# Performance work log

Measured on AMD Instinct MI355X. Metric: run time of the kernel, lower is better.

## Reference

```python
import jax, jax.numpy as jnp
import numpy as np

B, S, INP, HID = 64, 2048, 512, 512

def setup_inputs() -> dict:
    key = jax.random.key(0)
    ks = jax.random.split(key, 8)
    inp = jax.random.normal(ks[0], (B, INP), dtype=jnp.float32)
    context = jax.random.normal(ks[1], (B, S, INP), dtype=jnp.float32)
    mask = jax.random.randint(ks[2], (B, S), 0, 2) == 1  # True = masked out
    lim_l = 1.0 / np.sqrt(INP)
    Wl = jax.random.uniform(ks[3], (HID, INP), minval=-lim_l, maxval=lim_l, dtype=jnp.float32)
    bl = jax.random.uniform(ks[4], (HID,), minval=-lim_l, maxval=lim_l, dtype=jnp.float32)
    Wc = jax.random.uniform(ks[5], (HID, INP), minval=-lim_l, maxval=lim_l, dtype=jnp.float32)  # Conv1d k=1 weight squeezed
    bc = jax.random.uniform(ks[6], (HID,), minval=-lim_l, maxval=lim_l, dtype=jnp.float32)
    V = jax.random.uniform(ks[7], (HID,), minval=-1.0, maxval=1.0, dtype=jnp.float32)
    return {"inp": inp, "context": context, "mask": mask,
            "Wl": Wl, "bl": bl, "Wc": Wc, "bc": bc, "V": V}

def reference(inp, context, mask, Wl, bl, Wc, bc, V):
    # hid: [B, HID], broadcast over S
    hid = inp @ Wl.T + bl
    # 1x1 Conv1d over permuted context == per-position linear: [B, HID, S]
    ctx = jnp.einsum('bsi,hi->bhs', context, Wc) + bc[None, :, None]
    # additive attention scores: [B, S]
    att = jnp.einsum('h,bhs->bs', V, jnp.tanh(hid[:, :, None] + ctx))
    att = jnp.where(mask, -jnp.inf, att)
    alpha = jax.nn.softmax(att, axis=1)
    # context vector: [B, HID]
    hidden_state = jnp.einsum('bhs,bs->bh', ctx, alpha)
    return (hidden_state, alpha)
```

## Files before the change

kernel.cpp:

```cpp
#include <hip/hip_runtime.h>
#include <hip/hip_bf16.h>
#include <cstdint>
#include <cstddef>

#define B_   64
#define S_   2048
#define INP_ 512
#define HID_ 512

typedef float          floatx4  __attribute__((ext_vector_type(4)));
typedef __bf16         bf16x8   __attribute__((ext_vector_type(8)));
typedef unsigned short ushortx8 __attribute__((ext_vector_type(8)));
typedef unsigned short ushortx4 __attribute__((ext_vector_type(4)));

__device__ __forceinline__ unsigned short f2bf(float f) {
  unsigned u = __float_as_uint(f);
  u += 0x7FFFu + ((u >> 16) & 1u);
  return (unsigned short)(u >> 16);
}
__device__ __forceinline__ float bf2f(unsigned short h) {
  return __uint_as_float(((unsigned)h) << 16);
}
__device__ __forceinline__ float fast_tanh(float x) {
  float u = __builtin_amdgcn_exp2f(x * 2.88539008177792681472f);
  return 1.0f - 2.0f * __builtin_amdgcn_rcpf(u + 1.0f);
}

__global__ void hid_kernel(const float* __restrict__ inp, const float* __restrict__ Wl,
                           const float* __restrict__ bl, float* __restrict__ hid)
{
  __shared__ float ism[512];
  const int b = blockIdx.x, t = threadIdx.x;
  ism[t]       = inp[b * 512 + t];
  ism[t + 256] = inp[b * 512 + 256 + t];
  __syncthreads();
  #pragma unroll
  for (int hh = 0; hh < 2; ++hh) {
    int h = t + hh * 256;
    const float4* wr = (const float4*)(Wl + (size_t)h * 512);
    float4 sv = {0.f, 0.f, 0.f, 0.f};
    for (int i = 0; i < 128; ++i) {
      float4 wv = wr[i];
      float4 iv = *(const float4*)(&ism[i * 4]);
      sv.x += wv.x * iv.x; sv.y += wv.y * iv.y;
      sv.z += wv.z * iv.z; sv.w += wv.w * iv.w;
    }
    hid[b * 512 + h] = bl[h] + sv.x + sv.y + sv.z + sv.w;
  }
}

__global__ void pack_wc_kernel(const float* __restrict__ Wc, unsigned short* __restrict__ pk)
{
  int g = blockIdx.x * 256 + threadIdx.x;
  int l = g & 63, ks = (g >> 6) & 15, m16 = g >> 10;
  int row = m16 * 16 + (l & 15);
  int kb  = ks * 32 + (l >> 4) * 8;
  const float4* s = (const float4*)(Wc + (size_t)row * 512 + kb);
  float4 a = s[0], c = s[1];
  ushortx8 o = { f2bf(a.x), f2bf(a.y), f2bf(a.z), f2bf(a.w),
                 f2bf(c.x), f2bf(c.y), f2bf(c.z), f2bf(c.w) };
  *(ushortx8*)(pk + (size_t)g * 8) = o;
}

template<int MODE>
__global__ __launch_bounds__(256, 2) void ctx_gemm_kernel(
    const float* __restrict__ context, const unsigned short* __restrict__ Wc_pk,
    const float* __restrict__ hid, const float* __restrict__ bc,
    const float* __restrict__ V,
    unsigned short* __restrict__ ctx_out, float* __restrict__ att,
    const float* __restrict__ alpha, float* __restrict__ hidden)
{
  __shared__ alignas(16) unsigned short bsm[64 * 128];
  __shared__ float hid_sm[512];
  __shared__ float V_sm[512];
  __shared__ float bc_sm[512];
  __shared__ float att_sm[64];
  __shared__ float alpha_sm[64];

  const int b    = blockIdx.y;
  const int s0   = blockIdx.x * 64;
  const int t    = threadIdx.x;
  const int lane = t & 63;
  const int w    = t >> 6;
  const int quad = lane >> 4;
  const int l15  = lane & 15;

  for (int i = t; i < 512; i += 256) {
    hid_sm[i] = hid[b * 512 + i];
    V_sm[i]   = V[i];
    bc_sm[i]  = bc[i];
  }
  if (t < 64) {
    att_sm[t] = 0.0f;
    if (MODE == 2) alpha_sm[t] = alpha[b * S_ + s0 + t];
  }

  floatx4 acc[8][4];
  #pragma unroll
  for (int m = 0; m < 8; ++m)
    #pragma unroll
    for (int n = 0; n < 4; ++n) { floatx4 z = {0.f,0.f,0.f,0.f}; acc[m][n] = z; }

  const unsigned short* apBase = Wc_pk + (size_t)(w * 8) * 8192 + lane * 8;
  const float* src = context + ((size_t)b * S_ + s0) * INP_;

  for (int phase = 0; phase < 4; ++phase) {
    __syncthreads();
    #pragma unroll
    for (int i = 0; i < 8; ++i) {
      int id  = t + i * 256;
      int row = id >> 5;
      int c4  = id & 31;
      float4 f = *(const float4*)(src + (size_t)row * INP_ + phase * 128 + c4 * 4);
      int chunk = c4 >> 1, half = c4 & 1;
      int sw = chunk ^ (row & 7);
      ushortx4 hv = { f2bf(f.x), f2bf(f.y), f2bf(f.z), f2bf(f.w) };
      *(ushortx4*)(&bsm[row * 128 + sw * 8 + half * 4]) = hv;
    }
    __syncthreads();
    #pragma unroll
    for (int ksl = 0; ksl < 4; ++ksl) {
      const int ksg = phase * 4 + ksl;
      bf16x8 af[8];
      #pragma unroll
      for (int m = 0; m < 8; ++m)
        af[m] = *(const bf16x8*)(apBase + (size_t)m * 8192 + ksg * 512);
      bf16x8 bfr[4];
      #pragma unroll
      for (int n = 0; n < 4; ++n) {
        int row = n * 16 + l15;
        int c   = ksl * 4 + quad;
        bfr[n] = *(const bf16x8*)(&bsm[row * 128 + ((c ^ (row & 7)) * 8)]);
      }
      #pragma unroll
      for (int m = 0; m < 8; ++m)
        #pragma unroll
        for (int n = 0; n < 4; ++n)
          acc[m][n] = __builtin_amdgcn_mfma_f32_16x16x32_bf16(af[m], bfr[n], acc[m][n], 0, 0, 0);
    }
  }

  if (MODE == 0 || MODE == 1) {
    float attacc[4] = {0.f, 0.f, 0.f, 0.f};
    #pragma unroll
    for (int m = 0; m < 8; ++m) {
      int hb = w * 128 + m * 16 + quad * 4;
      #pragma unroll
      for (int r = 0; r < 4; ++r) {
        int h = hb + r;
        float bcv = bc_sm[h], hv = hid_sm[h], vv = V_sm[h];
        #pragma unroll
        for (int n = 0; n < 4; ++n) {
          float val = acc[m][n][r] + bcv;
          if (MODE == 0)
            ctx_out[((size_t)b * HID_ + h) * S_ + s0 + n * 16 + l15] = f2bf(val);
          attacc[n] += vv * fast_tanh(hv + val);
        }
      }
    }
    #pragma unroll
    for (int n = 0; n < 4; ++n) {
      float v = attacc[n];
      v += __shfl_xor(v, 16);
      v += __shfl_xor(v, 32);
      if (lane < 16) atomicAdd(&att_sm[n * 16 + l15], v);
    }
    __syncthreads();
    if (t < 64) att[b * S_ + s0 + t] = att_sm[t];
  } else {
    #pragma unroll
    for (int m = 0; m < 8; ++m) {
      int hb = w * 128 + m * 16 + quad * 4;
      #pragma unroll
      for (int r = 0; r < 4; ++r) {
        int h = hb + r;
        float bcv = bc_sm[h];
        float hacc = 0.0f;
        #pragma unroll
        for (int n = 0; n < 4; ++n)
          hacc += (acc[m][n][r] + bcv) * alpha_sm[n * 16 + l15];
        hacc += __shfl_xor(hacc, 1);
        hacc += __shfl_xor(hacc, 2);
        hacc += __shfl_xor(hacc, 4);
        hacc += __shfl_xor(hacc, 8);
        if (l15 == 0) atomicAdd(&hidden[b * HID_ + h], hacc);
      }
    }
  }
}

__global__ void softmax_kernel(const void* __restrict__ mask,
                               const float* __restrict__ att,
                               float* __restrict__ alpha)
{
  __shared__ int flags;
  __shared__ float red[8];
  const int b = blockIdx.x, t = threadIdx.x;
  const int lane = t & 63, w = t >> 6;
  if (t == 0) flags = 0;
  __syncthreads();
  int f = 0;
  const unsigned* mw = (const unsigned*)mask;
  for (int i = t; i < 512; i += 256) {
    unsigned v = mw[i];
    if (v > 1u) f |= 1;
    if (v != 0u && v != 0x3f800000u) f |= 2;
  }
  if (f) atomicOr(&flags, f);
  __syncthreads();
  const int fl = flags;
  const int mode = ((fl & 1) == 0) ? 0 : (((fl & 2) == 0) ? 1 : 2);

  float v[8]; bool msk[8];
  float vmax = -1e30f;
  #pragma unroll
  for (int i = 0; i < 8; ++i) {
    int idx = i * 256 + t;
    bool m;
    if (mode == 0)      m = ((const int*)mask)[b * S_ + idx] != 0;
    else if (mode == 1) m = ((const float*)mask)[b * S_ + idx] != 0.0f;
    else                m = ((const unsigned char*)mask)[b * S_ + idx] != 0;
    msk[i] = m;
    v[i] = att[b * S_ + idx];
    if (!m) vmax = fmaxf(vmax, v[i]);
  }
  #pragma unroll
  for (int off = 32; off; off >>= 1) vmax = fmaxf(vmax, __shfl_xor(vmax, off));
  if (lane == 0) red[w] = vmax;
  __syncthreads();
  vmax = fmaxf(fmaxf(red[0], red[1]), fmaxf(red[2], red[3]));

  float e[8], s = 0.0f;
  #pragma unroll
  for (int i = 0; i < 8; ++i) {
    e[i] = msk[i] ? 0.0f : __builtin_amdgcn_exp2f((v[i] - vmax) * 1.4426950408889634f);
    s += e[i];
  }
  #pragma unroll
  for (int off = 32; off; off >>= 1) s += __shfl_xor(s, off);
  if (lane == 0) red[4 + w] = s;
  __syncthreads();
  s = red[4] + red[5] + red[6] + red[7];
  float rinv = 1.0f / s;
  #pragma unroll
  for (int i = 0; i < 8; ++i)
    alpha[b * S_ + i * 256 + t] = e[i] * rinv;
}

__global__ void hidden_kernel(const unsigned short* __restrict__ ctx,
                              const float* __restrict__ alpha,
                              float* __restrict__ hidden)
{
  const int b = blockIdx.y;
  const int w = threadIdx.x >> 6, lane = threadIdx.x & 63;
  const int h = blockIdx.x * 4 + w;
  const unsigned short* cp = ctx + ((size_t)b * HID_ + h) * S_;
  const float* ap = alpha + (size_t)b * S_;
  float acc = 0.0f;
  #pragma unroll
  for (int it = 0; it < 4; ++it) {
    int s = it * 512 + lane * 8;
    ushortx8 cv = *(const ushortx8*)(cp + s);
    float4 a0 = *(const float4*)(ap + s);
    float4 a1 = *(const float4*)(ap + s + 4);
    acc += bf2f(cv[0]) * a0.x + bf2f(cv[1]) * a0.y + bf2f(cv[2]) * a0.z + bf2f(cv[3]) * a0.w
         + bf2f(cv[4]) * a1.x + bf2f(cv[5]) * a1.y + bf2f(cv[6]) * a1.z + bf2f(cv[7]) * a1.w;
  }
  #pragma unroll
  for (int off = 32; off; off >>= 1) acc += __shfl_xor(acc, off);
  if (lane == 0) hidden[b * HID_ + h] = acc;
}

extern "C" void kernel_launch(void* const* d_in, const int* in_sizes, int n_in,
                              void* d_out, int out_size, void* d_ws, size_t ws_size,
                              hipStream_t stream)
{
  const float* inp     = (const float*)d_in[0];
  const float* context = (const float*)d_in[1];
  const void*  mask    = d_in[2];
  const float* Wl      = (const float*)d_in[3];
  const float* bl      = (const float*)d_in[4];
  const float* Wc      = (const float*)d_in[5];
  const float* bc      = (const float*)d_in[6];
  const float* V       = (const float*)d_in[7];

  float* hidden = (float*)d_out;
  float* alpha  = (float*)d_out + B_ * HID_;

  char* ws = (char*)d_ws;
  const size_t CTX_BYTES = (size_t)B_ * HID_ * S_ * 2;
  const size_t HIDW_BYTES = (size_t)B_ * HID_ * 4;
  const size_t ATT_BYTES  = (size_t)B_ * S_ * 4;
  const size_t PK_BYTES   = (size_t)HID_ * INP_ * 2;
  const bool big = ws_size >= CTX_BYTES + HIDW_BYTES + ATT_BYTES + PK_BYTES;

  if (big) {
    unsigned short* ctx_bf = (unsigned short*)ws;
    float* hid_ws          = (float*)(ws + CTX_BYTES);
    float* att_ws          = (float*)(ws + CTX_BYTES + HIDW_BYTES);
    unsigned short* pk     = (unsigned short*)(ws + CTX_BYTES + HIDW_BYTES + ATT_BYTES);

    hid_kernel<<<B_, 256, 0, stream>>>(inp, Wl, bl, hid_ws);
    pack_wc_kernel<<<128, 256, 0, stream>>>(Wc, pk);
    ctx_gemm_kernel<0><<<dim3(S_ / 64, B_), 256, 0, stream>>>(
        context, pk, hid_ws, bc, V, ctx_bf, att_ws, nullptr, nullptr);
    softmax_kernel<<<B_, 256, 0, stream>>>(mask, att_ws, alpha);
    hidden_kernel<<<dim3(HID_ / 4, B_), 256, 0, stream>>>(ctx_bf, alpha, hidden);
  } else {
    float* hid_ws      = (float*)ws;
    float* att_ws      = (float*)(ws + HIDW_BYTES);
    unsigned short* pk = (unsigned short*)(ws + HIDW_BYTES + ATT_BYTES);

    hid_kernel<<<B_, 256, 0, stream>>>(inp, Wl, bl, hid_ws);
    pack_wc_kernel<<<128, 256, 0, stream>>>(Wc, pk);
    ctx_gemm_kernel<1><<<dim3(S_ / 64, B_), 256, 0, stream>>>(
        context, pk, hid_ws, bc, V, nullptr, att_ws, nullptr, nullptr);
    softmax_kernel<<<B_, 256, 0, stream>>>(mask, att_ws, alpha);
    hipMemsetAsync(hidden, 0, HIDW_BYTES, stream);
    ctx_gemm_kernel<2><<<dim3(S_ / 64, B_), 256, 0, stream>>>(
        context, pk, hid_ws, bc, V, nullptr, nullptr, alpha, hidden);
  }
}
```

Baseline: 518.3 us.

## Reassociate hidden-state as Wc·(context·alpha) and load context via LDS DMA

Uses linearity to compute hidden = Wc·(Σ_s alpha_s·context_s) + bc, since alpha sums to one. A new cbar kernel computes the alpha-weighted context average in fp32 partial chunks, and a rowdot kernel then applies Wc plus bias. This removes the need to write and reread the full bf16 ctx tensor or rerun the GEMM. The attention GEMM now loads fp32 context straight into LDS with global_load_lds and converts to bf16 at fragment-read time; it also streams A fragments per m to cut register use. The costs are a doubled LDS footprint for the tile, which may lower occupancy, and a second full read of context.

```diff
diff --git a/kernel.cpp b/kernel.cpp
--- a/kernel.cpp
+++ b/kernel.cpp
@@ -11,41 +11,57 @@
 typedef float          floatx4  __attribute__((ext_vector_type(4)));
 typedef __bf16         bf16x8   __attribute__((ext_vector_type(8)));
 typedef unsigned short ushortx8 __attribute__((ext_vector_type(8)));
-typedef unsigned short ushortx4 __attribute__((ext_vector_type(4)));
 
 __device__ __forceinline__ unsigned short f2bf(float f) {
   unsigned u = __float_as_uint(f);
   u += 0x7FFFu + ((u >> 16) & 1u);
   return (unsigned short)(u >> 16);
 }
-__device__ __forceinline__ float bf2f(unsigned short h) {
-  return __uint_as_float(((unsigned)h) << 16);
-}
 __device__ __forceinline__ float fast_tanh(float x) {
   float u = __builtin_amdgcn_exp2f(x * 2.88539008177792681472f);
   return 1.0f - 2.0f * __builtin_amdgcn_rcpf(u + 1.0f);
 }
 
-__global__ void hid_kernel(const float* __restrict__ inp, const float* __restrict__ Wl,
-                           const float* __restrict__ bl, float* __restrict__ hid)
-{
-  __shared__ float ism[512];
-  const int b = blockIdx.x, t = threadIdx.x;
-  ism[t]       = inp[b * 512 + t];
-  ism[t + 256] = inp[b * 512 + 256 + t];
-  __syncthreads();
-  #pragma unroll
-  for (int hh = 0; hh < 2; ++hh) {
-    int h = t + hh * 256;
-    const float4* wr = (const float4*)(Wl + (size_t)h * 512);
-    float4 sv = {0.f, 0.f, 0.f, 0.f};
-    for (int i = 0; i < 128; ++i) {
-      float4 wv = wr[i];
-      float4 iv = *(const float4*)(&ism[i * 4]);
-      sv.x += wv.x * iv.x; sv.y += wv.y * iv.y;
-      sv.z += wv.z * iv.z; sv.w += wv.w * iv.w;
-    }
-    hid[b * 512 + h] = bl[h] + sv.x + sv.y + sv.z + sv.w;
+__device__ __forceinline__ void gload_lds16(const float* g, float* l) {
+  __builtin_amdgcn_global_load_lds(
+      (const __attribute__((address_space(1))) unsigned int*)(const void*)g,
+      (__attribute__((address_space(3))) unsigned int*)(void*)l, 16, 0, 0);
+}
+
+template<int NPART>
+__global__ __launch_bounds__(256) void rowdot_kernel(
+    const float* __restrict__ W, const float* __restrict__ bias,
+    const float* __restrict__ vecs, float* __restrict__ out, int nch)
+{
+  __shared__ float vs[512];
+  const int b = blockIdx.y, t = threadIdx.x;
+  const int w = t >> 6, lane = t & 63;
+  for (int i = t; i < 512; i += 256) {
+    float s;
+    if (NPART) {
+      s = 0.0f;
+      for (int c = 0; c < nch; ++c)
+        s += vecs[((size_t)c * B_ + b) * INP_ + i];
+    } else {
+      s = vecs[(size_t)b * 512 + i];
+    }
+    vs[i] = s;
+  }
+  __syncthreads();
+  float vl[8];
+  #pragma unroll
+  for (int j = 0; j < 8; ++j) vl[j] = vs[lane * 8 + j];
+  const int h0 = blockIdx.x * 64 + w * 16;
+  #pragma unroll
+  for (int i = 0; i < 16; ++i) {
+    const int h = h0 + i;
+    const float4* wr = (const float4*)(W + (size_t)h * 512 + lane * 8);
+    float4 w0 = wr[0], w1 = wr[1];
+    float d = w0.x*vl[0] + w0.y*vl[1] + w0.z*vl[2] + w0.w*vl[3]
+            + w1.x*vl[4] + w1.y*vl[5] + w1.z*vl[6] + w1.w*vl[7];
+    #pragma unroll
+    for (int off = 32; off; off >>= 1) d += __shfl_xor(d, off);
+    if (lane == 0) out[(size_t)b * 512 + h] = bias[h] + d;
   }
 }
 
@@ -62,20 +78,16 @@
   *(ushortx8*)(pk + (size_t)g * 8) = o;
 }
 
-template<int MODE>
-__global__ __launch_bounds__(256, 2) void ctx_gemm_kernel(
+__global__ __launch_bounds__(256, 2) void att_gemm_kernel(
     const float* __restrict__ context, const unsigned short* __restrict__ Wc_pk,
     const float* __restrict__ hid, const float* __restrict__ bc,
-    const float* __restrict__ V,
-    unsigned short* __restrict__ ctx_out, float* __restrict__ att,
-    const float* __restrict__ alpha, float* __restrict__ hidden)
-{
-  __shared__ alignas(16) unsigned short bsm[64 * 128];
+    const float* __restrict__ V, float* __restrict__ att)
+{
+  __shared__ alignas(16) float bsf[64 * 128];
   __shared__ float hid_sm[512];
   __shared__ float V_sm[512];
   __shared__ float bc_sm[512];
   __shared__ float att_sm[64];
-  __shared__ float alpha_sm[64];
 
   const int b    = blockIdx.y;
   const int s0   = blockIdx.x * 64;
@@ -90,10 +102,7 @@
     V_sm[i]   = V[i];
     bc_sm[i]  = bc[i];
   }
-  if (t < 64) {
-    att_sm[t] = 0.0f;
-    if (MODE == 2) alpha_sm[t] = alpha[b * S_ + s0 + t];
-  }
+  if (t < 64) att_sm[t] = 0.0f;
 
   floatx4 acc[8][4];
   #pragma unroll
@@ -108,85 +117,64 @@
     __syncthreads();
     #pragma unroll
     for (int i = 0; i < 8; ++i) {
-      int id  = t + i * 256;
-      int row = id >> 5;
-      int c4  = id & 31;
-      float4 f = *(const float4*)(src + (size_t)row * INP_ + phase * 128 + c4 * 4);
-      int chunk = c4 >> 1, half = c4 & 1;
-      int sw = chunk ^ (row & 7);
-      ushortx4 hv = { f2bf(f.x), f2bf(f.y), f2bf(f.z), f2bf(f.w) };
-      *(ushortx4*)(&bsm[row * 128 + sw * 8 + half * 4]) = hv;
+      const int row = (w * 8 + i) * 2 + (lane >> 5);
+      const int c   = (lane & 31) ^ (row & 7);
+      gload_lds16(src + (size_t)row * INP_ + phase * 128 + c * 4,
+                  &bsf[(w * 8 + i) * 256]);
     }
     __syncthreads();
     #pragma unroll
     for (int ksl = 0; ksl < 4; ++ksl) {
       const int ksg = phase * 4 + ksl;
-      bf16x8 af[8];
-      #pragma unroll
-      for (int m = 0; m < 8; ++m)
-        af[m] = *(const bf16x8*)(apBase + (size_t)m * 8192 + ksg * 512);
       bf16x8 bfr[4];
       #pragma unroll
       for (int n = 0; n < 4; ++n) {
-        int row = n * 16 + l15;
-        int c   = ksl * 4 + quad;
-        bfr[n] = *(const bf16x8*)(&bsm[row * 128 + ((c ^ (row & 7)) * 8)]);
+        const int row = n * 16 + l15;
+        const int cb  = ksl * 8 + quad * 2;
+        const int p0  = cb ^ (row & 7);
+        const int p1  = (cb + 1) ^ (row & 7);
+        floatx4 f0 = *(const floatx4*)(&bsf[row * 128 + p0 * 4]);
+        floatx4 f1 = *(const floatx4*)(&bsf[row * 128 + p1 * 4]);
+        bf16x8 r;
+        r[0] = (__bf16)f0[0]; r[1] = (__bf16)f0[1];
+        r[2] = (__bf16)f0[2]; r[3] = (__bf16)f0[3];
+        r[4] = (__bf16)f1[0]; r[5] = (__bf16)f1[1];
+        r[6] = (__bf16)f1[2]; r[7] = (__bf16)f1[3];
+        bfr[n] = r;
       }
       #pragma unroll
-      for (int m = 0; m < 8; ++m)
+      for (int m = 0; m < 8; ++m) {
+        bf16x8 af = *(const bf16x8*)(apBase + (size_t)m * 8192 + (size_t)ksg * 512);
         #pragma unroll
         for (int n = 0; n < 4; ++n)
-          acc[m][n] = __builtin_amdgcn_mfma_f32_16x16x32_bf16(af[m], bfr[n], acc[m][n], 0, 0, 0);
-    }
-  }
-
-  if (MODE == 0 || MODE == 1) {
-    float attacc[4] = {0.f, 0.f, 0.f, 0.f};
-    #pragma unroll
-    for (int m = 0; m < 8; ++m) {
-      int hb = w * 128 + m * 16 + quad * 4;
+          acc[m][n] = __builtin_amdgcn_mfma_f32_16x16x32_bf16(af, bfr[n], acc[m][n], 0, 0, 0);
+      }
+    }
+  }
+
+  float attacc[4] = {0.f, 0.f, 0.f, 0.f};
+  #pragma unroll
+  for (int m = 0; m < 8; ++m) {
+    const int hb = w * 128 + m * 16 + quad * 4;
+    #pragma unroll
+    for (int r = 0; r < 4; ++r) {
+      const int h = hb + r;
+      const float base = hid_sm[h] + bc_sm[h];
+      const float vv = V_sm[h];
       #pragma unroll
-      for (int r = 0; r < 4; ++r) {
-        int h = hb + r;
-        float bcv = bc_sm[h], hv = hid_sm[h], vv = V_sm[h];
-        #pragma unroll
-        for (int n = 0; n < 4; ++n) {
-          float val = acc[m][n][r] + bcv;
-          if (MODE == 0)
-            ctx_out[((size_t)b * HID_ + h) * S_ + s0 + n * 16 + l15] = f2bf(val);
-          attacc[n] += vv * fast_tanh(hv + val);
-        }
-      }
-    }
-    #pragma unroll
-    for (int n = 0; n < 4; ++n) {
-      float v = attacc[n];
-      v += __shfl_xor(v, 16);
-      v += __shfl_xor(v, 32);
-      if (lane < 16) atomicAdd(&att_sm[n * 16 + l15], v);
-    }
-    __syncthreads();
-    if (t < 64) att[b * S_ + s0 + t] = att_sm[t];
-  } else {
-    #pragma unroll
-    for (int m = 0; m < 8; ++m) {
-      int hb = w * 128 + m * 16 + quad * 4;
-      #pragma unroll
-      for (int r = 0; r < 4; ++r) {
-        int h = hb + r;
-        float bcv = bc_sm[h];
-        float hacc = 0.0f;
-        #pragma unroll
-        for (int n = 0; n < 4; ++n)
-          hacc += (acc[m][n][r] + bcv) * alpha_sm[n * 16 + l15];
-        hacc += __shfl_xor(hacc, 1);
-        hacc += __shfl_xor(hacc, 2);
-        hacc += __shfl_xor(hacc, 4);
-        hacc += __shfl_xor(hacc, 8);
-        if (l15 == 0) atomicAdd(&hidden[b * HID_ + h], hacc);
-      }
-    }
-  }
+      for (int n = 0; n < 4; ++n)
+        attacc[n] += vv * fast_tanh(base + acc[m][n][r]);
+    }
+  }
+  #pragma unroll
+  for (int n = 0; n < 4; ++n) {
+    float v = attacc[n];
+    v += __shfl_xor(v, 16);
+    v += __shfl_xor(v, 32);
+    if (lane < 16) atomicAdd(&att_sm[n * 16 + l15], v);
+  }
+  __syncthreads();
+  if (t < 64) att[b * S_ + s0 + t] = att_sm[t];
 }
 
 __global__ void softmax_kernel(const void* __restrict__ mask,
@@ -247,28 +235,26 @@
     alpha[b * S_ + i * 256 + t] = e[i] * rinv;
 }
 
-__global__ void hidden_kernel(const unsigned short* __restrict__ ctx,
-                              const float* __restrict__ alpha,
-                              float* __restrict__ hidden)
-{
-  const int b = blockIdx.y;
-  const int w = threadIdx.x >> 6, lane = threadIdx.x & 63;
-  const int h = blockIdx.x * 4 + w;
-  const unsigned short* cp = ctx + ((size_t)b * HID_ + h) * S_;
-  const float* ap = alpha + (size_t)b * S_;
-  float acc = 0.0f;
-  #pragma unroll
-  for (int it = 0; it < 4; ++it) {
-    int s = it * 512 + lane * 8;
-    ushortx8 cv = *(const ushortx8*)(cp + s);
-    float4 a0 = *(const float4*)(ap + s);
-    float4 a1 = *(const float4*)(ap + s + 4);
-    acc += bf2f(cv[0]) * a0.x + bf2f(cv[1]) * a0.y + bf2f(cv[2]) * a0.z + bf2f(cv[3]) * a0.w
-         + bf2f(cv[4]) * a1.x + bf2f(cv[5]) * a1.y + bf2f(cv[6]) * a1.z + bf2f(cv[7]) * a1.w;
-  }
-  #pragma unroll
-  for (int off = 32; off; off >>= 1) acc += __shfl_xor(acc, off);
-  if (lane == 0) hidden[b * HID_ + h] = acc;
+__global__ __launch_bounds__(256) void cbar_kernel(
+    const float* __restrict__ context, const float* __restrict__ alpha,
+    float* __restrict__ partial, int rows)
+{
+  __shared__ float a_sm[2048];
+  const int b = blockIdx.y, c = blockIdx.x, t = threadIdx.x;
+  const int s0 = c * rows;
+  for (int i = t; i < rows; i += 256) a_sm[i] = alpha[(size_t)b * S_ + s0 + i];
+  __syncthreads();
+  const float* base = context + ((size_t)b * S_ + s0) * INP_ + t * 2;
+  float ax = 0.f, ay = 0.f;
+  #pragma unroll 8
+  for (int s = 0; s < rows; ++s) {
+    float2 v = *(const float2*)(base + (size_t)s * INP_);
+    float a = a_sm[s];
+    ax = fmaf(a, v.x, ax);
+    ay = fmaf(a, v.y, ay);
+  }
+  float2 o; o.x = ax; o.y = ay;
+  *(float2*)(partial + ((size_t)c * B_ + b) * INP_ + t * 2) = o;
 }
 
 extern "C" void kernel_launch(void* const* d_in, const int* in_sizes, int n_in,
@@ -288,36 +274,24 @@
   float* alpha  = (float*)d_out + B_ * HID_;
 
   char* ws = (char*)d_ws;
-  const size_t CTX_BYTES = (size_t)B_ * HID_ * S_ * 2;
   const size_t HIDW_BYTES = (size_t)B_ * HID_ * 4;
   const size_t ATT_BYTES  = (size_t)B_ * S_ * 4;
   const size_t PK_BYTES   = (size_t)HID_ * INP_ * 2;
-  const bool big = ws_size >= CTX_BYTES + HIDW_BYTES + ATT_BYTES + PK_BYTES;
-
-  if (big) {
-    unsigned short* ctx_bf = (unsigned short*)ws;
-    float* hid_ws          = (float*)(ws + CTX_BYTES);
-    float* att_ws          = (float*)(ws + CTX_BYTES + HIDW_BYTES);
-    unsigned short* pk     = (unsigned short*)(ws + CTX_BYTES + HIDW_BYTES + ATT_BYTES);
-
-    hid_kernel<<<B_, 256, 0, stream>>>(inp, Wl, bl, hid_ws);
-    pack_wc_kernel<<<128, 256, 0, stream>>>(Wc, pk);
-    ctx_gemm_kernel<0><<<dim3(S_ / 64, B_), 256, 0, stream>>>(
-        context, pk, hid_ws, bc, V, ctx_bf, att_ws, nullptr, nullptr);
-    softmax_kernel<<<B_, 256, 0, stream>>>(mask, att_ws, alpha);
-    hidden_kernel<<<dim3(HID_ / 4, B_), 256, 0, stream>>>(ctx_bf, alpha, hidden);
-  } else {
-    float* hid_ws      = (float*)ws;
-    float* att_ws      = (float*)(ws + HIDW_BYTES);
-    unsigned short* pk = (unsigned short*)(ws + HIDW_BYTES + ATT_BYTES);
-
-    hid_kernel<<<B_, 256, 0, stream>>>(inp, Wl, bl, hid_ws);
-    pack_wc_kernel<<<128, 256, 0, stream>>>(Wc, pk);
-    ctx_gemm_kernel<1><<<dim3(S_ / 64, B_), 256, 0, stream>>>(
-        context, pk, hid_ws, bc, V, nullptr, att_ws, nullptr, nullptr);
-    softmax_kernel<<<B_, 256, 0, stream>>>(mask, att_ws, alpha);
-    hipMemsetAsync(hidden, 0, HIDW_BYTES, stream);
-    ctx_gemm_kernel<2><<<dim3(S_ / 64, B_), 256, 0, stream>>>(
-        context, pk, hid_ws, bc, V, nullptr, nullptr, alpha, hidden);
-  }
-}
+
+  float* hid_ws      = (float*)ws;
+  float* att_ws      = (float*)(ws + HIDW_BYTES);
+  unsigned short* pk = (unsigned short*)(ws + HIDW_BYTES + ATT_BYTES);
+  float* partial     = (float*)(ws + HIDW_BYTES + ATT_BYTES + PK_BYTES);
+
+  const size_t rem = ws_size - (HIDW_BYTES + ATT_BYTES + PK_BYTES);
+  int nch = 16;
+  while (nch > 1 && (size_t)nch * B_ * INP_ * 4 > rem) nch >>= 1;
+  const int rows = S_ / nch;
+
+  rowdot_kernel<0><<<dim3(HID_ / 64, B_), 256, 0, stream>>>(Wl, bl, inp, hid_ws, 0);
+  pack_wc_kernel<<<128, 256, 0, stream>>>(Wc, pk);
+  att_gemm_kernel<<<dim3(S_ / 64, B_), 256, 0, stream>>>(context, pk, hid_ws, bc, V, att_ws);
+  softmax_kernel<<<B_, 256, 0, stream>>>(mask, att_ws, alpha);
+  cbar_kernel<<<dim3(nch, B_), 256, 0, stream>>>(context, alpha, partial, rows);
+  rowdot_kernel<1><<<dim3(HID_ / 64, B_), 256, 0, stream>>>(Wc, bc, partial, hidden, nch);
+}
```

After: 551.2 us. 1.06x slower.
